# Kernel optimization log

Measured on AMD Instinct MI355X. Metric: run time of the kernel, lower is better.

Reference implementation:

```python
import jax, jax.numpy as jnp
import numpy as np

N, K, D = 524288, 64, 2
EPS = 1e-6
LOG_2PI = float(np.log(2.0 * np.pi))


def setup_inputs() -> dict:
    key = jax.random.key(0)
    k1, k2, k3, k4 = jax.random.split(key, 4)
    x = jax.random.normal(k1, (N, D), dtype=jnp.float32) * 2.0
    means = jax.random.normal(k2, (K, D), dtype=jnp.float32)
    # cholesky factor param: identity plus small noise (tril applied in forward)
    chol_var = jnp.eye(D, dtype=jnp.float32)[None] + 0.1 * jax.random.normal(k3, (K, D, D), dtype=jnp.float32)
    pi = jax.random.uniform(k4, (K,), dtype=jnp.float32)
    return {"x": x, "means": means, "chol_var": chol_var, "pi": pi}


def reference(x, means, chol_var, pi):
    # x: [N, D]; means: [K, D]; chol_var: [K, D, D]; pi: [K]
    K_, D_ = means.shape
    L = jnp.tril(chol_var)                                   # [K, D, D]
    cov = L @ jnp.swapaxes(L, -1, -2) + EPS * jnp.eye(D_, dtype=x.dtype)
    chol = jnp.linalg.cholesky(cov)                          # [K, D, D] lower
    logdet = 2.0 * jnp.sum(jnp.log(jnp.diagonal(chol, axis1=-2, axis2=-1)), axis=-1)  # [K]
    cinv = jnp.linalg.inv(chol)                              # [K, D, D] (tiny DxD)
    diff = x[:, None, :] - means[None, :, :]                 # [N, K, D]
    y = jnp.einsum('kij,nkj->nki', cinv, diff)               # whitened residuals
    quad = jnp.sum(y * y, axis=-1)                           # [N, K] Mahalanobis^2
    log_probs = -0.5 * (D_ * LOG_2PI + logdet[None, :] + quad)  # [N, K]
    weighted = log_probs + jax.nn.log_softmax(pi)            # [N, K]
    return jax.nn.logsumexp(weighted, axis=1)                # [N]
```

## Files before the change

### kernel.cpp

```cpp
#include <hip/hip_runtime.h>
#include <hip/hip_bf16.h>
#include <math.h>
#include <stdint.h>

#define LOG_2PI_D 1.837877066409345483560659472811
#define LOG2E_D   1.442695040888963407359924681002
#define LN2_F     0.69314718055994530942f

typedef const float __attribute__((address_space(4))) cfloat;

__global__ __launch_bounds__(256, 2) void gmm_fused(
        const float* __restrict__ x,
        const float* __restrict__ means,
        const float* __restrict__ chol_var,
        const float* __restrict__ pi,
        float* __restrict__ out,
        float* scratch,
        int n2) {
    const int tid = threadIdx.x;
    const int bid = blockIdx.x;

    if (tid < 64) {
        const int k = tid;
        float p = pi[k];
        float mx = p;
        #pragma unroll
        for (int off = 32; off > 0; off >>= 1) mx = fmaxf(mx, __shfl_xor(mx, off, 64));
        float sf = __expf(p - mx);
        #pragma unroll
        for (int off = 32; off > 0; off >>= 1) sf += __shfl_xor(sf, off, 64);
        double logpi = (double)p - (double)mx - (double)__logf(sf);

        double v00 = (double)chol_var[k*4 + 0];
        double v10 = (double)chol_var[k*4 + 2];
        double v11 = (double)chol_var[k*4 + 3];
        const double eps = 1e-6;
        double cov00 = v00*v00 + eps;
        double cov01 = v00*v10;
        double cov11 = v10*v10 + v11*v11 + eps;
        double a  = sqrt(cov00);
        double b  = cov01 / a;
        double c2 = cov11 - b*b;
        double logdet = (double)__logf((float)(cov00 * c2));
        double P00 = 1.0/cov00 + (b*b)/(cov00*c2);
        double P01 = -b/(a*c2);
        double P11 = 1.0/c2;
        double m0 = (double)means[k*2 + 0];
        double m1 = (double)means[k*2 + 1];
        double constk = -0.5*(2.0*LOG_2PI_D + logdet) + logpi;

        scratch[k*6 + 0] = (float)(-0.5*P00*LOG2E_D);
        scratch[k*6 + 1] = (float)(-P01*LOG2E_D);
        scratch[k*6 + 2] = (float)(-0.5*P11*LOG2E_D);
        scratch[k*6 + 3] = (float)((P00*m0 + P01*m1)*LOG2E_D);
        scratch[k*6 + 4] = (float)((P01*m0 + P11*m1)*LOG2E_D);
        scratch[k*6 + 5] = (float)((constk
                        - 0.5*(P00*m0*m0 + 2.0*P01*m0*m1 + P11*m1*m1))*LOG2E_D);
        asm volatile("s_waitcnt vmcnt(0)" ::: "memory");
    }
    __syncthreads();

    const float* cp = scratch;
    asm volatile("" : "+s"(cp) :: "memory");
    cfloat* cc = (cfloat*)(uintptr_t)cp;

    int i = bid * 256 + tid;
    if (i >= n2) return;

    float4 xv = reinterpret_cast<const float4*>(x)[i];
    float a00 = xv.x*xv.x, a01 = xv.x*xv.y, a11 = xv.y*xv.y;
    float b00 = xv.z*xv.z, b01 = xv.z*xv.w, b11 = xv.w*xv.w;

    float wa[64], wb[64];
    float ma = -INFINITY, mb = -INFINITY;
    #pragma unroll
    for (int k = 0; k < 64; ++k) {
        float C0 = cc[k*6+0], C1 = cc[k*6+1], C2 = cc[k*6+2];
        float C3 = cc[k*6+3], C4 = cc[k*6+4], C5 = cc[k*6+5];
        float ta = C5, tb = C5;
        ta = fmaf(C0, a00, ta);   tb = fmaf(C0, b00, tb);
        ta = fmaf(C1, a01, ta);   tb = fmaf(C1, b01, tb);
        ta = fmaf(C2, a11, ta);   tb = fmaf(C2, b11, tb);
        ta = fmaf(C3, xv.x, ta);  tb = fmaf(C3, xv.z, tb);
        ta = fmaf(C4, xv.y, ta);  tb = fmaf(C4, xv.w, tb);
        wa[k] = ta;  wb[k] = tb;
        ma = fmaxf(ma, ta);  mb = fmaxf(mb, tb);
    }

    float sa0 = 0.f, sa1 = 0.f, sb0 = 0.f, sb1 = 0.f;
    #pragma unroll
    for (int k = 0; k < 64; k += 2) {
        sa0 += __builtin_amdgcn_exp2f(wa[k]   - ma);
        sa1 += __builtin_amdgcn_exp2f(wa[k+1] - ma);
        sb0 += __builtin_amdgcn_exp2f(wb[k]   - mb);
        sb1 += __builtin_amdgcn_exp2f(wb[k+1] - mb);
    }
    float2 o;
    o.x = LN2_F * (ma + __builtin_amdgcn_logf(sa0 + sa1));
    o.y = LN2_F * (mb + __builtin_amdgcn_logf(sb0 + sb1));
    reinterpret_cast<float2*>(out)[i] = o;
}

extern "C" void kernel_launch(void* const* d_in, const int* in_sizes, int n_in,
                              void* d_out, int out_size, void* d_ws, size_t ws_size,
                              hipStream_t stream) {
    const float* x        = (const float*)d_in[0];
    const float* means    = (const float*)d_in[1];
    const float* chol_var = (const float*)d_in[2];
    const float* pi       = (const float*)d_in[3];
    float* out     = (float*)d_out;
    float* scratch = (float*)d_ws;

    int n  = in_sizes[0] / 2;
    int n2 = n / 2;
    int blocks = (n2 + 255) / 256;

    gmm_fused<<<blocks, 256, 0, stream>>>(x, means, chol_var, pi, out, scratch, n2);
}
```

Before: 73.21 us.

## Compute per-component constants in every wave and broadcast via readlane; use packed FMA

Every wave now computes the 64 per-component quadratic coefficients itself, one component per lane. This drops the single-wave scratch write, the vmcnt wait, the __syncthreads barrier and the scalar-memory reload. The coefficients are broadcast to all lanes with readlane, and the two points per thread are evaluated with 2-wide vector FMA/max so the compiler can emit packed fp32 instructions. The cost is redundant double-precision setup math in every wave and 384 readlanes per wave.

```diff
diff --git a/kernel.cpp b/kernel.cpp
--- a/kernel.cpp
+++ b/kernel.cpp
@@ -7,7 +7,12 @@
 #define LOG2E_D   1.442695040888963407359924681002
 #define LN2_F     0.69314718055994530942f
 
-typedef const float __attribute__((address_space(4))) cfloat;
+typedef float v2f __attribute__((ext_vector_type(2)));
+
+__device__ __forceinline__ float rl(float v, int l) {
+    return __builtin_bit_cast(float,
+        __builtin_amdgcn_readlane(__builtin_bit_cast(int, v), l));
+}
 
 __global__ __launch_bounds__(256, 2) void gmm_fused(
         const float* __restrict__ x,
@@ -15,89 +20,86 @@
         const float* __restrict__ chol_var,
         const float* __restrict__ pi,
         float* __restrict__ out,
-        float* scratch,
         int n2) {
-    const int tid = threadIdx.x;
-    const int bid = blockIdx.x;
+    const int lane = threadIdx.x & 63;
 
-    if (tid < 64) {
-        const int k = tid;
-        float p = pi[k];
-        float mx = p;
-        #pragma unroll
-        for (int off = 32; off > 0; off >>= 1) mx = fmaxf(mx, __shfl_xor(mx, off, 64));
-        float sf = __expf(p - mx);
-        #pragma unroll
-        for (int off = 32; off > 0; off >>= 1) sf += __shfl_xor(sf, off, 64);
-        double logpi = (double)p - (double)mx - (double)__logf(sf);
+    {
+    }
+    const int k = lane;
+    float p = pi[k];
+    float mx = p;
+    #pragma unroll
+    for (int off = 32; off > 0; off >>= 1) mx = fmaxf(mx, __shfl_xor(mx, off, 64));
+    float sf = __expf(p - mx);
+    #pragma unroll
+    for (int off = 32; off > 0; off >>= 1) sf += __shfl_xor(sf, off, 64);
+    double logpi = (double)p - (double)mx - (double)__logf(sf);
 
-        double v00 = (double)chol_var[k*4 + 0];
-        double v10 = (double)chol_var[k*4 + 2];
-        double v11 = (double)chol_var[k*4 + 3];
-        const double eps = 1e-6;
-        double cov00 = v00*v00 + eps;
-        double cov01 = v00*v10;
-        double cov11 = v10*v10 + v11*v11 + eps;
-        double a  = sqrt(cov00);
-        double b  = cov01 / a;
-        double c2 = cov11 - b*b;
-        double logdet = (double)__logf((float)(cov00 * c2));
-        double P00 = 1.0/cov00 + (b*b)/(cov00*c2);
-        double P01 = -b/(a*c2);
-        double P11 = 1.0/c2;
-        double m0 = (double)means[k*2 + 0];
-        double m1 = (double)means[k*2 + 1];
-        double constk = -0.5*(2.0*LOG_2PI_D + logdet) + logpi;
+    double v00 = (double)chol_var[k*4 + 0];
+    double v10 = (double)chol_var[k*4 + 2];
+    double v11 = (double)chol_var[k*4 + 3];
+    const double eps = 1e-6;
+    double cov00 = v00*v00 + eps;
+    double cov01 = v00*v10;
+    double cov11 = v10*v10 + v11*v11 + eps;
+    double a  = sqrt(cov00);
+    double b  = cov01 / a;
+    double c2 = cov11 - b*b;
+    double logdet = (double)__logf((float)(cov00 * c2));
+    double P00 = 1.0/cov00 + (b*b)/(cov00*c2);
+    double P01 = -b/(a*c2);
+    double P11 = 1.0/c2;
+    double m0 = (double)means[k*2 + 0];
+    double m1 = (double)means[k*2 + 1];
+    double constk = -0.5*(2.0*LOG_2PI_D + logdet) + logpi;
 
-        scratch[k*6 + 0] = (float)(-0.5*P00*LOG2E_D);
-        scratch[k*6 + 1] = (float)(-P01*LOG2E_D);
-        scratch[k*6 + 2] = (float)(-0.5*P11*LOG2E_D);
-        scratch[k*6 + 3] = (float)((P00*m0 + P01*m1)*LOG2E_D);
-        scratch[k*6 + 4] = (float)((P01*m0 + P11*m1)*LOG2E_D);
-        scratch[k*6 + 5] = (float)((constk
-                        - 0.5*(P00*m0*m0 + 2.0*P01*m0*m1 + P11*m1*m1))*LOG2E_D);
-        asm volatile("s_waitcnt vmcnt(0)" ::: "memory");
-    }
-    __syncthreads();
+    float C0 = (float)(-0.5*P00*LOG2E_D);
+    float C1 = (float)(-P01*LOG2E_D);
+    float C2 = (float)(-0.5*P11*LOG2E_D);
+    float C3 = (float)((P00*m0 + P01*m1)*LOG2E_D);
+    float C4 = (float)((P01*m0 + P11*m1)*LOG2E_D);
+    float C5 = (float)((constk
+                 - 0.5*(P00*m0*m0 + 2.0*P01*m0*m1 + P11*m1*m1))*LOG2E_D);
 
-    const float* cp = scratch;
-    asm volatile("" : "+s"(cp) :: "memory");
-    cfloat* cc = (cfloat*)(uintptr_t)cp;
-
-    int i = bid * 256 + tid;
+    int i = blockIdx.x * 256 + threadIdx.x;
     if (i >= n2) return;
 
     float4 xv = reinterpret_cast<const float4*>(x)[i];
-    float a00 = xv.x*xv.x, a01 = xv.x*xv.y, a11 = xv.y*xv.y;
-    float b00 = xv.z*xv.z, b01 = xv.z*xv.w, b11 = xv.w*xv.w;
+    v2f X0  = { xv.x, xv.z };
+    v2f X1  = { xv.y, xv.w };
+    v2f Q00 = X0 * X0;
+    v2f Q01 = X0 * X1;
+    v2f Q11 = X1 * X1;
 
-    float wa[64], wb[64];
-    float ma = -INFINITY, mb = -INFINITY;
+    v2f w2[64];
+    v2f m2 = { -INFINITY, -INFINITY };
     #pragma unroll
-    for (int k = 0; k < 64; ++k) {
-        float C0 = cc[k*6+0], C1 = cc[k*6+1], C2 = cc[k*6+2];
-        float C3 = cc[k*6+3], C4 = cc[k*6+4], C5 = cc[k*6+5];
-        float ta = C5, tb = C5;
-        ta = fmaf(C0, a00, ta);   tb = fmaf(C0, b00, tb);
-        ta = fmaf(C1, a01, ta);   tb = fmaf(C1, b01, tb);
-        ta = fmaf(C2, a11, ta);   tb = fmaf(C2, b11, tb);
-        ta = fmaf(C3, xv.x, ta);  tb = fmaf(C3, xv.z, tb);
-        ta = fmaf(C4, xv.y, ta);  tb = fmaf(C4, xv.w, tb);
-        wa[k] = ta;  wb[k] = tb;
-        ma = fmaxf(ma, ta);  mb = fmaxf(mb, tb);
+    for (int kk = 0; kk < 64; ++kk) {
+        float c0 = rl(C0, kk), c1 = rl(C1, kk), c2f = rl(C2, kk);
+        float c3 = rl(C3, kk), c4 = rl(C4, kk), c5 = rl(C5, kk);
+        v2f t = { c5, c5 };
+        t = __builtin_elementwise_fma((v2f){c0, c0}, Q00, t);
+        t = __builtin_elementwise_fma((v2f){c1, c1}, Q01, t);
+        t = __builtin_elementwise_fma((v2f){c2f, c2f}, Q11, t);
+        t = __builtin_elementwise_fma((v2f){c3, c3}, X0,  t);
+        t = __builtin_elementwise_fma((v2f){c4, c4}, X1,  t);
+        w2[kk] = t;
+        m2 = __builtin_elementwise_max(m2, t);
     }
 
     float sa0 = 0.f, sa1 = 0.f, sb0 = 0.f, sb1 = 0.f;
     #pragma unroll
-    for (int k = 0; k < 64; k += 2) {
-        sa0 += __builtin_amdgcn_exp2f(wa[k]   - ma);
-        sa1 += __builtin_amdgcn_exp2f(wa[k+1] - ma);
-        sb0 += __builtin_amdgcn_exp2f(wb[k]   - mb);
-        sb1 += __builtin_amdgcn_exp2f(wb[k+1] - mb);
+    for (int kk = 0; kk < 64; kk += 2) {
+        v2f d0 = w2[kk]     - m2;
+        v2f d1 = w2[kk + 1] - m2;
+        sa0 += __builtin_amdgcn_exp2f(d0.x);
+        sb0 += __builtin_amdgcn_exp2f(d0.y);
+        sa1 += __builtin_amdgcn_exp2f(d1.x);
+        sb1 += __builtin_amdgcn_exp2f(d1.y);
     }
     float2 o;
-    o.x = LN2_F * (ma + __builtin_amdgcn_logf(sa0 + sa1));
-    o.y = LN2_F * (mb + __builtin_amdgcn_logf(sb0 + sb1));
+    o.x = LN2_F * (m2.x + __builtin_amdgcn_logf(sa0 + sa1));
+    o.y = LN2_F * (m2.y + __builtin_amdgcn_logf(sb0 + sb1));
     reinterpret_cast<float2*>(out)[i] = o;
 }
 
@@ -108,12 +110,11 @@
     const float* means    = (const float*)d_in[1];
     const float* chol_var = (const float*)d_in[2];
     const float* pi       = (const float*)d_in[3];
-    float* out     = (float*)d_out;
-    float* scratch = (float*)d_ws;
+    float* out = (float*)d_out;
 
     int n  = in_sizes[0] / 2;
     int n2 = n / 2;
     int blocks = (n2 + 255) / 256;
 
-    gmm_fused<<<blocks, 256, 0, stream>>>(x, means, chol_var, pi, out, scratch, n2);
+    gmm_fused<<<blocks, 256, 0, stream>>>(x, means, chol_var, pi, out, n2);
 }
```

Result: faster. 71.40 us (-2.5%).
